# Kernel optimization log

Hardware: AMD Instinct MI355X
Metric: run time of the kernel (lower is better)

The kernel has to match this reference:

```python
import jax, jax.numpy as jnp
import numpy as np

EMBED_DIM = 512
K = 30
B, M, L = 64, 1024, 256

def setup_inputs() -> dict:
    key = jax.random.key(0)
    ks = jax.random.split(key, 7)
    s = 0.05  # small scale so tanh/softmax stay in a sane numeric range
    return {
        "V": jax.random.normal(ks[0], (B, EMBED_DIM, M), dtype=jnp.float32),
        "Q": jax.random.normal(ks[1], (B, L, EMBED_DIM), dtype=jnp.float32),
        "W_b": jax.random.normal(ks[2], (EMBED_DIM, EMBED_DIM), dtype=jnp.float32) * s,
        "W_v": jax.random.normal(ks[3], (K, EMBED_DIM), dtype=jnp.float32) * s,
        "W_q": jax.random.normal(ks[4], (K, EMBED_DIM), dtype=jnp.float32) * s,
        "w_hv": jax.random.normal(ks[5], (K, 1), dtype=jnp.float32) * s,
        "w_hq": jax.random.normal(ks[6], (K, 1), dtype=jnp.float32) * s,
    }

def reference(V, Q, W_b, W_v, W_q, w_hv, w_hq):
    # V: [B, d, M], Q: [B, L, d]
    b, d, m = V.shape
    l = Q.shape[1]
    WbV = jnp.einsum('de,bem->bdm', W_b, V)          # [B, d, M]
    C = jnp.matmul(Q, WbV)                            # affinity [B, L, M]
    WvV = jnp.einsum('kd,bdm->bkm', W_v, V)           # [B, k, M]
    WqQ = jnp.einsum('kd,bld->bkl', W_q, Q)           # [B, k, L]
    H_v = jnp.tanh(WvV + jnp.matmul(WqQ, C))          # [B, k, M]
    H_q = jnp.tanh(WqQ + jnp.matmul(WvV, jnp.swapaxes(C, 1, 2)))  # [B, k, L]
    a_v = jax.nn.softmax(jnp.einsum('ko,bkm->bom', w_hv, H_v), axis=2)  # [B, 1, M]
    a_q = jax.nn.softmax(jnp.einsum('ko,bkl->bol', w_hq, H_q), axis=2)  # [B, 1, L]
    # torch stacks a_v M times then matmuls -> M identical pooled rows; compute
    # the pooled vector once and broadcast (same math, no [B,M,M] intermediate).
    v1 = jnp.matmul(a_v, jnp.swapaxes(V, 1, 2))       # [B, 1, d]
    q1 = jnp.matmul(a_q, Q)                           # [B, 1, d]
    v = jnp.broadcast_to(v1, (b, m, d))               # [B, M, d]
    q = jnp.broadcast_to(q1, (b, l, d))               # [B, L, d]
    return (v, q)
```

## Files before the change

### kernel.cpp

```cpp
#include <hip/hip_runtime.h>

constexpr int Bn = 64;
constexpr int Dn = 512;
constexpr int Mn = 1024;
constexpr int Ln = 256;
constexpr int Kn = 30;
constexpr int KP = 32;

typedef __attribute__((ext_vector_type(4))) float f32x4;
typedef __attribute__((ext_vector_type(2))) float f32x2;
typedef __attribute__((ext_vector_type(4))) unsigned int u32x4;
typedef __attribute__((ext_vector_type(8))) _Float16 f16x8;
typedef __attribute__((ext_vector_type(2))) _Float16 f16x2;
typedef unsigned short ushort_t;

__device__ __forceinline__ void cvt_pair(float a, float b,
                                         unsigned int& hp, unsigned int& lp)
{
    _Float16 ha = (_Float16)a, hb = (_Float16)b;
    _Float16 la = (_Float16)(a - (float)ha), lb = (_Float16)(b - (float)hb);
    f16x2 hv = {ha, hb}, lv = {la, lb};
    hp = __builtin_bit_cast(unsigned int, hv);
    lp = __builtin_bit_cast(unsigned int, lv);
}

__device__ __forceinline__ unsigned int cvt_one_pack(float x)
{
    _Float16 h = (_Float16)x;
    _Float16 l = (_Float16)(x - (float)h);
    return (unsigned int)__builtin_bit_cast(ushort_t, l) |
           ((unsigned int)__builtin_bit_cast(ushort_t, h) << 16);
}

template <int MT, bool BT, int EPI>
__global__ __launch_bounds__(256) void fgemm_kernel(
    const float* __restrict__ A, const float* __restrict__ B,
    float* __restrict__ C,
    const float* __restrict__ Wvec, const float* __restrict__ Xadd,
    float* __restrict__ Yout,
    int Mreal, int Ndim, int Kdim, int ldA, int ldB,
    long sA, long sB, long sC)
{
    constexpr int BM = MT * 16;
    constexpr int AP = 20;
    constexpr int ASZ = BM * AP;
    constexpr int BP_NN = 66;
    constexpr int BSZ = BT ? (2 * 64 * AP) : (32 * BP_NN);
    __shared__ unsigned int smem[2 * ASZ + BSZ];
    __shared__ float wsh[32];
    unsigned int* Ah = smem;
    unsigned int* Al = smem + ASZ;
    unsigned int* Bh = smem + 2 * ASZ;
    unsigned int* Bl = Bh + 64 * AP;
    unsigned int* Bp = smem + 2 * ASZ;

    const int t  = threadIdx.x;
    const int n0 = blockIdx.x * 64;
    const int m0 = blockIdx.y * BM;
    const int b  = blockIdx.z;
    const float* Ab = A + (long)b * sA;
    const float* Bb = B + (long)b * sB;

    const int lane = t & 63, w = t >> 6;
    const int fr = lane & 15, g = lane >> 4;
    const int kp  = t & 15, r16 = t >> 4;
    const int nn  = t & 63, kr  = t >> 6;

    if (EPI >= 2 && t < 32) wsh[t] = (t < Kn) ? Wvec[t] : 0.f;

    float as[MT][2];
    float bsv[8];

    auto stageA = [&](int k0) {
        #pragma unroll
        for (int i = 0; i < MT; i++) {
            int gm = m0 + r16 + 16 * i;
            float x0 = 0.f, x1 = 0.f;
            if (gm < Mreal) {
                f32x2 v = *(const f32x2*)&Ab[(long)gm * ldA + k0 + 2 * kp];
                x0 = v.x; x1 = v.y;
            }
            as[i][0] = x0; as[i][1] = x1;
        }
    };
    auto stageB = [&](int k0) {
        if constexpr (BT) {
            #pragma unroll
            for (int i = 0; i < 4; i++) {
                f32x2 v = *(const f32x2*)&Bb[(long)(n0 + r16 + 16 * i) * ldB + k0 + 2 * kp];
                bsv[2 * i] = v.x; bsv[2 * i + 1] = v.y;
            }
        } else {
            #pragma unroll
            for (int i = 0; i < 8; i++)
                bsv[i] = Bb[(long)(k0 + kr + 4 * i) * ldB + n0 + nn];
        }
    };
    auto storeStage = [&]() {
        #pragma unroll
        for (int i = 0; i < MT; i++) {
            unsigned int hp, lp;
            cvt_pair(as[i][0], as[i][1], hp, lp);
            Ah[(r16 + 16 * i) * AP + kp] = hp;
            Al[(r16 + 16 * i) * AP + kp] = lp;
        }
        if constexpr (BT) {
            #pragma unroll
            for (int i = 0; i < 4; i++) {
                unsigned int hp, lp;
                cvt_pair(bsv[2 * i], bsv[2 * i + 1], hp, lp);
                Bh[(r16 + 16 * i) * AP + kp] = hp;
                Bl[(r16 + 16 * i) * AP + kp] = lp;
            }
        } else {
            #pragma unroll
            for (int i = 0; i < 8; i++)
                Bp[(kr + 4 * i) * BP_NN + nn] = cvt_one_pack(bsv[i]);
        }
    };

    f32x4 acc[MT];
    #pragma unroll
    for (int i = 0; i < MT; i++) acc[i] = (f32x4){0.f, 0.f, 0.f, 0.f};

    auto computeTile = [&]() {
        f16x8 fbh, fbl;
        if constexpr (BT) {
            int row = w * 16 + fr;
            fbh = __builtin_bit_cast(f16x8, *(const u32x4*)&Bh[row * AP + g * 4]);
            fbl = __builtin_bit_cast(f16x8, *(const u32x4*)&Bl[row * AP + g * 4]);
        } else {
            unsigned int p[8];
            #pragma unroll
            for (int j = 0; j < 8; j++)
                p[j] = Bp[(g * 8 + j) * BP_NN + w * 16 + fr];
            unsigned int hu[4], lu[4];
            #pragma unroll
            for (int r = 0; r < 4; r++) {
                hu[r] = __builtin_amdgcn_perm(p[2 * r + 1], p[2 * r], 0x07060302u);
                lu[r] = __builtin_amdgcn_perm(p[2 * r + 1], p[2 * r], 0x05040100u);
            }
            fbh = __builtin_bit_cast(f16x8, (u32x4){hu[0], hu[1], hu[2], hu[3]});
            fbl = __builtin_bit_cast(f16x8, (u32x4){lu[0], lu[1], lu[2], lu[3]});
        }
        #pragma unroll
        for (int mt = 0; mt < MT; mt++) {
            int row = fr + 16 * mt;
            f16x8 fah = __builtin_bit_cast(f16x8, *(const u32x4*)&Ah[row * AP + g * 4]);
            f16x8 fal = __builtin_bit_cast(f16x8, *(const u32x4*)&Al[row * AP + g * 4]);
            acc[mt] = __builtin_amdgcn_mfma_f32_16x16x32_f16(fah, fbh, acc[mt], 0, 0, 0);
            acc[mt] = __builtin_amdgcn_mfma_f32_16x16x32_f16(fal, fbh, acc[mt], 0, 0, 0);
            acc[mt] = __builtin_amdgcn_mfma_f32_16x16x32_f16(fah, fbl, acc[mt], 0, 0, 0);
        }
    };

    stageA(0); stageB(0);
    storeStage();
    __syncthreads();
    const int nt = Kdim >> 5;
    for (int tt = 0; tt < nt; tt++) {
        const bool more = (tt + 1 < nt);
        if (more) { stageA((tt + 1) * 32); stageB((tt + 1) * 32); }
        computeTile();
        if (more) {
            __syncthreads();
            storeStage();
            __syncthreads();
        }
    }

    const int col = n0 + w * 16 + fr;
    if constexpr (EPI == 0) {
        float* Cb = C + (long)b * sC;
        #pragma unroll
        for (int mt = 0; mt < MT; mt++)
            #pragma unroll
            for (int r = 0; r < 4; r++)
                Cb[(long)(m0 + mt * 16 + g * 4 + r) * Ndim + col] = acc[mt][r];
    } else if constexpr (EPI == 1) {
        #pragma unroll
        for (int mt = 0; mt < MT; mt++)
            #pragma unroll
            for (int r = 0; r < 4; r++) {
                int gr = m0 + mt * 16 + g * 4 + r;
                int sr = (gr >> 5) * 64 + 32 + (gr & 31);
                C[(long)sr * Ndim + col] = acc[mt][r];
            }
    } else if constexpr (EPI == 2) {
        float* Cb = C + (long)b * sC;
        float s = 0.f;
        #pragma unroll
        for (int mt = 0; mt < 2; mt++)
            #pragma unroll
            for (int r = 0; r < 4; r++) {
                int row = mt * 16 + g * 4 + r;
                Cb[(long)row * Ndim + col] = acc[mt][r];
                s += wsh[row] * tanhf(acc[mt][r] + acc[mt + 2][r]);
            }
        s += __shfl_xor(s, 16, 64);
        s += __shfl_xor(s, 32, 64);
        if (g == 0) Yout[(long)b * Ndim + col] = s;
    } else {
        const float* Xb = Xadd + (long)b * sC;
        float s = 0.f;
        #pragma unroll
        for (int mt = 0; mt < MT; mt++)
            #pragma unroll
            for (int r = 0; r < 4; r++) {
                int row = mt * 16 + g * 4 + r;
                s += wsh[row] * tanhf(Xb[(long)row * Ndim + col] + acc[mt][r]);
            }
        s += __shfl_xor(s, 16, 64);
        s += __shfl_xor(s, 32, 64);
        if (g == 0) Yout[(long)b * Ndim + col] = s;
    }
}

__global__ void prep_sa_kernel(const float* __restrict__ Wv,
                               float* __restrict__ Sa)
{
    const int b = blockIdx.x, t = threadIdx.x;
    for (int idx = t; idx < 32 * Dn; idx += 256) {
        int row = idx >> 9, col = idx & 511;
        Sa[((long)b * 64 + row) * Dn + col] =
            (row < Kn) ? Wv[(long)row * Dn + col] : 0.f;
    }
}

__global__ __launch_bounds__(1024) void smpool_v_kernel(
    const float* __restrict__ sv, const float* __restrict__ V,
    float* __restrict__ v1)
{
    const int b = blockIdx.y, qtr = blockIdx.x, t = threadIdx.x;
    const int wid = t >> 6, lane = t & 63;
    __shared__ float red[16];
    __shared__ float bc;
    __shared__ float av[Mn];

    float x = sv[(long)b * Mn + t];
    float v = x;
    #pragma unroll
    for (int off = 32; off > 0; off >>= 1) v = fmaxf(v, __shfl_down(v, off, 64));
    if (lane == 0) red[wid] = v;
    __syncthreads();
    if (t == 0) {
        float m = red[0];
        for (int i = 1; i < 16; i++) m = fmaxf(m, red[i]);
        bc = m;
    }
    __syncthreads();
    float e = expf(x - bc);
    v = e;
    #pragma unroll
    for (int off = 32; off > 0; off >>= 1) v += __shfl_down(v, off, 64);
    if (lane == 0) red[wid] = v;
    __syncthreads();
    if (t == 0) {
        float s = 0.f;
        for (int i = 0; i < 16; i++) s += red[i];
        bc = s;
    }
    __syncthreads();
    av[t] = e / bc;
    __syncthreads();

    f32x4 aa[4];
    #pragma unroll
    for (int i = 0; i < 4; i++) aa[i] = *(const f32x4*)&av[4 * (lane + 64 * i)];

    #pragma unroll
    for (int j = 0; j < 8; j++) {
        int e_ = qtr * 128 + wid * 8 + j;
        const float* vr = V + ((long)b * Dn + e_) * Mn;
        float acc = 0.f;
        #pragma unroll
        for (int i = 0; i < 4; i++) {
            f32x4 vv = *(const f32x4*)&vr[4 * (lane + 64 * i)];
            acc += vv.x * aa[i].x + vv.y * aa[i].y + vv.z * aa[i].z + vv.w * aa[i].w;
        }
        #pragma unroll
        for (int off = 32; off > 0; off >>= 1) acc += __shfl_down(acc, off, 64);
        if (lane == 0) v1[(long)b * Dn + e_] = acc;
    }
}

__global__ __launch_bounds__(256) void smpool_q_kernel(
    const float* __restrict__ sq, const float* __restrict__ Q,
    float* __restrict__ q1)
{
    const int b = blockIdx.y, half = blockIdx.x, t = threadIdx.x;
    const int wid = t >> 6, lane = t & 63;
    __shared__ float red[4];
    __shared__ float bc;
    __shared__ float aq[Ln];

    float x = sq[(long)b * Ln + t];
    float v = x;
    #pragma unroll
    for (int off = 32; off > 0; off >>= 1) v = fmaxf(v, __shfl_down(v, off, 64));
    if (lane == 0) red[wid] = v;
    __syncthreads();
    if (t == 0) {
        float m = red[0];
        for (int i = 1; i < 4; i++) m = fmaxf(m, red[i]);
        bc = m;
    }
    __syncthreads();
    float e = expf(x - bc);
    v = e;
    #pragma unroll
    for (int off = 32; off > 0; off >>= 1) v += __shfl_down(v, off, 64);
    if (lane == 0) red[wid] = v;
    __syncthreads();
    if (t == 0) {
        float s = 0.f;
        for (int i = 0; i < 4; i++) s += red[i];
        bc = s;
    }
    __syncthreads();
    aq[t] = e / bc;
    __syncthreads();

    const int e_ = half * 256 + t;
    const float* Qb = Q + (long)b * Ln * Dn;
    float acc = 0.f;
    #pragma unroll 4
    for (int l = 0; l < Ln; l++)
        acc += aq[l] * Qb[(long)l * Dn + e_];
    q1[(long)b * Dn + e_] = acc;
}

__global__ void bcast_kernel(const float* __restrict__ v1,
                             const float* __restrict__ q1,
                             float* __restrict__ out)
{
    const long nv4 = (long)Bn * Mn * Dn / 4;
    const long nq4 = (long)Bn * Ln * Dn / 4;
    long idx = (long)blockIdx.x * blockDim.x + threadIdx.x;
    float4* o4 = (float4*)out;
    if (idx < nv4) {
        long fidx = idx * 4;
        int e4 = (int)(fidx & (Dn - 1));
        long bm = fidx >> 9;
        int b = (int)(bm >> 10);
        o4[idx] = *(const float4*)(v1 + (long)b * Dn + e4);
    } else if (idx < nv4 + nq4) {
        long fidx = (idx - nv4) * 4;
        int e4 = (int)(fidx & (Dn - 1));
        long bl = fidx >> 9;
        int b = (int)(bl >> 8);
        o4[idx] = *(const float4*)(q1 + (long)b * Dn + e4);
    }
}


extern "C" void kernel_launch(void* const* d_in, const int* in_sizes, int n_in,
                              void* d_out, int out_size, void* d_ws, size_t ws_size,
                              hipStream_t stream)
{
    const float* V    = (const float*)d_in[0];
    const float* Q    = (const float*)d_in[1];
    const float* W_b  = (const float*)d_in[2];
    const float* W_v  = (const float*)d_in[3];
    const float* W_q  = (const float*)d_in[4];
    const float* w_hv = (const float*)d_in[5];
    const float* w_hq = (const float*)d_in[6];
    float* out = (float*)d_out;

    const long szWqQ = (long)Bn * KP * Ln;
    const long szU   = (long)Bn * KP * Dn;
    const long szSa  = (long)Bn * 64 * Dn;
    const long szSo  = (long)Bn * 32 * Mn;

    float* ws   = (float*)d_ws;
    float* WqQ  = ws;
    float* U    = WqQ + szWqQ;
    float* Sa   = U   + szU;
    float* Sout = Sa  + szSa;
    float* R    = Sout + szSo;
    float* G    = R   + szU;
    float* sv   = G   + szU;
    float* sq   = sv  + (long)Bn * Mn;
    float* v1   = sq  + (long)Bn * Ln;
    float* q1   = v1  + (long)Bn * Dn;

    prep_sa_kernel<<<Bn, 256, 0, stream>>>(W_v, Sa);

    fgemm_kernel<2, true, 0><<<dim3(Ln / 64, 1, Bn), 256, 0, stream>>>(
        W_q, Q, WqQ, nullptr, nullptr, nullptr,
        Kn, Ln, Dn, Dn, Dn, 0, (long)Ln * Dn, (long)KP * Ln);

    fgemm_kernel<2, false, 0><<<dim3(Dn / 64, 1, Bn), 256, 0, stream>>>(
        WqQ, Q, U, nullptr, nullptr, nullptr,
        KP, Dn, Ln, Ln, Dn, (long)KP * Ln, (long)Ln * Dn, (long)KP * Dn);

    fgemm_kernel<4, false, 1><<<dim3(Dn / 64, Bn * KP / 64, 1), 256, 0, stream>>>(
        U, W_b, Sa, nullptr, nullptr, nullptr,
        Bn * KP, Dn, Dn, Dn, Dn, 0, 0, 0);

    fgemm_kernel<4, false, 2><<<dim3(Mn / 64, 1, Bn), 256, 0, stream>>>(
        Sa, V, Sout, w_hv, nullptr, sv,
        64, Mn, Dn, Dn, Mn, (long)64 * Dn, (long)Dn * Mn, (long)32 * Mn);

    fgemm_kernel<2, true, 0><<<dim3(Dn / 64, 1, Bn), 256, 0, stream>>>(
        Sout, V, R, nullptr, nullptr, nullptr,
        KP, Dn, Mn, Mn, Mn, (long)32 * Mn, (long)Dn * Mn, (long)KP * Dn);

    fgemm_kernel<4, true, 0><<<dim3(Dn / 64, Bn * KP / 64, 1), 256, 0, stream>>>(
        R, W_b, G, nullptr, nullptr, nullptr,
        Bn * KP, Dn, Dn, Dn, Dn, 0, 0, 0);

    fgemm_kernel<2, true, 3><<<dim3(Ln / 64, 1, Bn), 256, 0, stream>>>(
        G, Q, nullptr, w_hq, WqQ, sq,
        KP, Ln, Dn, Dn, Dn, (long)KP * Dn, (long)Ln * Dn, (long)KP * Ln);

    smpool_v_kernel<<<dim3(4, Bn), 1024, 0, stream>>>(sv, V, v1);

    smpool_q_kernel<<<dim3(2, Bn), 256, 0, stream>>>(sq, Q, q1);

    {
        long n4 = (long)Bn * Mn * Dn / 4 + (long)Bn * Ln * Dn / 4;
        bcast_kernel<<<(int)((n4 + 255) / 256), 256, 0, stream>>>(v1, q1, out);
    }
}
```

Baseline: 494.6 us.

## Pre-pack fp16 hi/lo operands, double-buffer LDS, and parallelize q pooling

```diff
diff --git a/kernel.cpp b/kernel.cpp
--- a/kernel.cpp
+++ b/kernel.cpp
@@ -10,9 +10,25 @@
 typedef __attribute__((ext_vector_type(4))) float f32x4;
 typedef __attribute__((ext_vector_type(2))) float f32x2;
 typedef __attribute__((ext_vector_type(4))) unsigned int u32x4;
+typedef __attribute__((ext_vector_type(2))) unsigned int u32x2;
 typedef __attribute__((ext_vector_type(8))) _Float16 f16x8;
 typedef __attribute__((ext_vector_type(2))) _Float16 f16x2;
 typedef unsigned short ushort_t;
+
+__device__ __forceinline__ unsigned int cvt_one_pack(float x)
+{
+    _Float16 h = (_Float16)x;
+    _Float16 l = (_Float16)(x - (float)h);
+    return (unsigned int)__builtin_bit_cast(ushort_t, l) |
+           ((unsigned int)__builtin_bit_cast(ushort_t, h) << 16);
+}
+
+__device__ __forceinline__ float unpacksplit(unsigned int p)
+{
+    _Float16 h = __builtin_bit_cast(_Float16, (ushort_t)(p >> 16));
+    _Float16 l = __builtin_bit_cast(_Float16, (ushort_t)(p & 0xffffu));
+    return (float)h + (float)l;
+}
 
 __device__ __forceinline__ void cvt_pair(float a, float b,
                                          unsigned int& hp, unsigned int& lp)
@@ -24,19 +40,37 @@
     lp = __builtin_bit_cast(unsigned int, lv);
 }
 
-__device__ __forceinline__ unsigned int cvt_one_pack(float x)
-{
-    _Float16 h = (_Float16)x;
-    _Float16 l = (_Float16)(x - (float)h);
-    return (unsigned int)__builtin_bit_cast(ushort_t, l) |
-           ((unsigned int)__builtin_bit_cast(ushort_t, h) << 16);
-}
-
-template <int MT, bool BT, int EPI>
+#define PERM_HI 0x07060302u
+#define PERM_LO 0x05040100u
+
+__global__ __launch_bounds__(256) void pack4_kernel(
+    const float* __restrict__ s0, unsigned int* __restrict__ d0, long n0,
+    const float* __restrict__ s1, unsigned int* __restrict__ d1, long n1,
+    const float* __restrict__ s2, unsigned int* __restrict__ d2, long n2,
+    const float* __restrict__ s3, unsigned int* __restrict__ d3, long n3)
+{
+    long total4 = (n0 + n1 + n2 + n3) >> 2;
+    long stride = (long)gridDim.x * blockDim.x;
+    for (long c = (long)blockIdx.x * blockDim.x + threadIdx.x; c < total4; c += stride) {
+        long i = c * 4;
+        const float* s; unsigned int* d; long off;
+        if (i < n0)                { s = s0; d = d0; off = i; }
+        else if (i < n0 + n1)      { s = s1; d = d1; off = i - n0; }
+        else if (i < n0 + n1 + n2) { s = s2; d = d2; off = i - n0 - n1; }
+        else                       { s = s3; d = d3; off = i - n0 - n1 - n2; }
+        f32x4 v = *(const f32x4*)(s + off);
+        u32x4 o = { cvt_one_pack(v.x), cvt_one_pack(v.y),
+                    cvt_one_pack(v.z), cvt_one_pack(v.w) };
+        *(u32x4*)(d + off) = o;
+    }
+}
+
+template <int MT, bool BT, int EPI, bool BPACK, int ASRC>
 __global__ __launch_bounds__(256) void fgemm_kernel(
-    const float* __restrict__ A, const float* __restrict__ B,
-    float* __restrict__ C,
-    const float* __restrict__ Wvec, const float* __restrict__ Xadd,
+    const unsigned int* __restrict__ A, const void* __restrict__ B,
+    const unsigned int* __restrict__ A2,
+    unsigned int* __restrict__ C,
+    const float* __restrict__ Wvec, const unsigned int* __restrict__ Xadd,
     float* __restrict__ Yout,
     int Mreal, int Ndim, int Kdim, int ldA, int ldB,
     long sA, long sB, long sC)
@@ -46,20 +80,17 @@
     constexpr int ASZ = BM * AP;
     constexpr int BP_NN = 66;
     constexpr int BSZ = BT ? (2 * 64 * AP) : (32 * BP_NN);
-    __shared__ unsigned int smem[2 * ASZ + BSZ];
+    constexpr int HALF = 2 * ASZ + BSZ;
+    __shared__ unsigned int smem[2 * HALF];
     __shared__ float wsh[32];
-    unsigned int* Ah = smem;
-    unsigned int* Al = smem + ASZ;
-    unsigned int* Bh = smem + 2 * ASZ;
-    unsigned int* Bl = Bh + 64 * AP;
-    unsigned int* Bp = smem + 2 * ASZ;
 
     const int t  = threadIdx.x;
     const int n0 = blockIdx.x * 64;
     const int m0 = blockIdx.y * BM;
     const int b  = blockIdx.z;
-    const float* Ab = A + (long)b * sA;
-    const float* Bb = B + (long)b * sB;
+    const unsigned int* Ab = A + (long)b * sA;
+    const float*        Bf = (const float*)B + (long)b * sB;
+    const unsigned int* Bu = (const unsigned int*)B + (long)b * sB;
 
     const int lane = t & 63, w = t >> 6;
     const int fr = lane & 15, g = lane >> 4;
@@ -68,54 +99,82 @@
 
     if (EPI >= 2 && t < 32) wsh[t] = (t < Kn) ? Wvec[t] : 0.f;
 
-    float as[MT][2];
-    float bsv[8];
+    unsigned int aA[MT][2];
+    unsigned int bu[8];
+    float bf[8];
 
     auto stageA = [&](int k0) {
         #pragma unroll
         for (int i = 0; i < MT; i++) {
             int gm = m0 + r16 + 16 * i;
-            float x0 = 0.f, x1 = 0.f;
-            if (gm < Mreal) {
-                f32x2 v = *(const f32x2*)&Ab[(long)gm * ldA + k0 + 2 * kp];
-                x0 = v.x; x1 = v.y;
-            }
-            as[i][0] = x0; as[i][1] = x1;
+            unsigned int p0 = 0, p1 = 0;
+            if constexpr (ASRC == 2) {
+                if (gm < Kn) {
+                    u32x2 v = *(const u32x2*)&A[(long)gm * ldA + k0 + 2 * kp];
+                    p0 = v.x; p1 = v.y;
+                } else if (gm >= 32) {
+                    u32x2 v = *(const u32x2*)&A2[((long)b * 32 + gm - 32) * ldA + k0 + 2 * kp];
+                    p0 = v.x; p1 = v.y;
+                }
+            } else {
+                if (gm < Mreal) {
+                    u32x2 v = *(const u32x2*)&Ab[(long)gm * ldA + k0 + 2 * kp];
+                    p0 = v.x; p1 = v.y;
+                }
+            }
+            aA[i][0] = p0; aA[i][1] = p1;
         }
     };
     auto stageB = [&](int k0) {
         if constexpr (BT) {
             #pragma unroll
             for (int i = 0; i < 4; i++) {
-                f32x2 v = *(const f32x2*)&Bb[(long)(n0 + r16 + 16 * i) * ldB + k0 + 2 * kp];
-                bsv[2 * i] = v.x; bsv[2 * i + 1] = v.y;
+                long off = (long)(n0 + r16 + 16 * i) * ldB + k0 + 2 * kp;
+                if constexpr (BPACK) {
+                    u32x2 v = *(const u32x2*)&Bu[off];
+                    bu[2 * i] = v.x; bu[2 * i + 1] = v.y;
+                } else {
+                    f32x2 v = *(const f32x2*)&Bf[off];
+                    bf[2 * i] = v.x; bf[2 * i + 1] = v.y;
+                }
             }
         } else {
             #pragma unroll
-            for (int i = 0; i < 8; i++)
-                bsv[i] = Bb[(long)(k0 + kr + 4 * i) * ldB + n0 + nn];
+            for (int i = 0; i < 8; i++) {
+                long off = (long)(k0 + kr + 4 * i) * ldB + n0 + nn;
+                if constexpr (BPACK) bu[i] = Bu[off];
+                else                 bf[i] = Bf[off];
+            }
         }
     };
-    auto storeStage = [&]() {
+    auto storeStage = [&](unsigned int* sm) {
+        unsigned int* Ah = sm;
+        unsigned int* Al = sm + ASZ;
         #pragma unroll
         for (int i = 0; i < MT; i++) {
-            unsigned int hp, lp;
-            cvt_pair(as[i][0], as[i][1], hp, lp);
-            Ah[(r16 + 16 * i) * AP + kp] = hp;
-            Al[(r16 + 16 * i) * AP + kp] = lp;
+            Ah[(r16 + 16 * i) * AP + kp] = __builtin_amdgcn_perm(aA[i][1], aA[i][0], PERM_HI);
+            Al[(r16 + 16 * i) * AP + kp] = __builtin_amdgcn_perm(aA[i][1], aA[i][0], PERM_LO);
         }
         if constexpr (BT) {
+            unsigned int* Bh = sm + 2 * ASZ;
+            unsigned int* Bl = Bh + 64 * AP;
             #pragma unroll
             for (int i = 0; i < 4; i++) {
                 unsigned int hp, lp;
-                cvt_pair(bsv[2 * i], bsv[2 * i + 1], hp, lp);
+                if constexpr (BPACK) {
+                    hp = __builtin_amdgcn_perm(bu[2 * i + 1], bu[2 * i], PERM_HI);
+                    lp = __builtin_amdgcn_perm(bu[2 * i + 1], bu[2 * i], PERM_LO);
+                } else {
+                    cvt_pair(bf[2 * i], bf[2 * i + 1], hp, lp);
+                }
                 Bh[(r16 + 16 * i) * AP + kp] = hp;
                 Bl[(r16 + 16 * i) * AP + kp] = lp;
             }
         } else {
+            unsigned int* Bp = sm + 2 * ASZ;
             #pragma unroll
             for (int i = 0; i < 8; i++)
-                Bp[(kr + 4 * i) * BP_NN + nn] = cvt_one_pack(bsv[i]);
+                Bp[(kr + 4 * i) * BP_NN + nn] = BPACK ? bu[i] : cvt_one_pack(bf[i]);
         }
     };
 
@@ -123,13 +182,18 @@
     #pragma unroll
     for (int i = 0; i < MT; i++) acc[i] = (f32x4){0.f, 0.f, 0.f, 0.f};
 
-    auto computeTile = [&]() {
+    auto computeTile = [&](const unsigned int* sm) {
+        const unsigned int* Ah = sm;
+        const unsigned int* Al = sm + ASZ;
         f16x8 fbh, fbl;
         if constexpr (BT) {
+            const unsigned int* Bh = sm + 2 * ASZ;
+            const unsigned int* Bl = Bh + 64 * AP;
             int row = w * 16 + fr;
             fbh = __builtin_bit_cast(f16x8, *(const u32x4*)&Bh[row * AP + g * 4]);
             fbl = __builtin_bit_cast(f16x8, *(const u32x4*)&Bl[row * AP + g * 4]);
         } else {
+            const unsigned int* Bp = sm + 2 * ASZ;
             unsigned int p[8];
             #pragma unroll
             for (int j = 0; j < 8; j++)
@@ -137,8 +201,8 @@
             unsigned int hu[4], lu[4];
             #pragma unroll
             for (int r = 0; r < 4; r++) {
-                hu[r] = __builtin_amdgcn_perm(p[2 * r + 1], p[2 * r], 0x07060302u);
-                lu[r] = __builtin_amdgcn_perm(p[2 * r + 1], p[2 * r], 0x05040100u);
+                hu[r] = __builtin_amdgcn_perm(p[2 * r + 1], p[2 * r], PERM_HI);
+                lu[r] = __builtin_amdgcn_perm(p[2 * r + 1], p[2 * r], PERM_LO);
             }
             fbh = __builtin_bit_cast(f16x8, (u32x4){hu[0], hu[1], hu[2], hu[3]});
             fbl = __builtin_bit_cast(f16x8, (u32x4){lu[0], lu[1], lu[2], lu[3]});
@@ -154,76 +218,56 @@
         }
     };
 
+    const int nt = Kdim >> 5;
     stageA(0); stageB(0);
-    storeStage();
-    __syncthreads();
-    const int nt = Kdim >> 5;
+    storeStage(smem);
+    __syncthreads();
     for (int tt = 0; tt < nt; tt++) {
+        unsigned int* cur = smem + (tt & 1) * HALF;
+        unsigned int* nxt = smem + ((tt + 1) & 1) * HALF;
         const bool more = (tt + 1 < nt);
-        if (more) { stageA((tt + 1) * 32); stageB((tt + 1) * 32); }
-        computeTile();
-        if (more) {
-            __syncthreads();
-            storeStage();
-            __syncthreads();
-        }
+        if (more) { stageA((tt + 1) << 5); stageB((tt + 1) << 5); }
+        computeTile(cur);
+        if (more) storeStage(nxt);
+        __syncthreads();
     }
 
     const int col = n0 + w * 16 + fr;
     if constexpr (EPI == 0) {
-        float* Cb = C + (long)b * sC;
+        unsigned int* Cb = C + (long)b * sC;
         #pragma unroll
         for (int mt = 0; mt < MT; mt++)
             #pragma unroll
             for (int r = 0; r < 4; r++)
-                Cb[(long)(m0 + mt * 16 + g * 4 + r) * Ndim + col] = acc[mt][r];
-    } else if constexpr (EPI == 1) {
-        #pragma unroll
-        for (int mt = 0; mt < MT; mt++)
-            #pragma unroll
-            for (int r = 0; r < 4; r++) {
-                int gr = m0 + mt * 16 + g * 4 + r;
-                int sr = (gr >> 5) * 64 + 32 + (gr & 31);
-                C[(long)sr * Ndim + col] = acc[mt][r];
-            }
+                Cb[(long)(m0 + mt * 16 + g * 4 + r) * Ndim + col] = cvt_one_pack(acc[mt][r]);
     } else if constexpr (EPI == 2) {
-        float* Cb = C + (long)b * sC;
+        unsigned int* Cb = C + (long)b * sC;
         float s = 0.f;
         #pragma unroll
         for (int mt = 0; mt < 2; mt++)
             #pragma unroll
             for (int r = 0; r < 4; r++) {
                 int row = mt * 16 + g * 4 + r;
-                Cb[(long)row * Ndim + col] = acc[mt][r];
+                Cb[(long)row * Ndim + col] = cvt_one_pack(acc[mt][r]);
                 s += wsh[row] * tanhf(acc[mt][r] + acc[mt + 2][r]);
             }
         s += __shfl_xor(s, 16, 64);
         s += __shfl_xor(s, 32, 64);
         if (g == 0) Yout[(long)b * Ndim + col] = s;
     } else {
-        const float* Xb = Xadd + (long)b * sC;
+        const unsigned int* Xb = Xadd + (long)b * sC;
         float s = 0.f;
         #pragma unroll
         for (int mt = 0; mt < MT; mt++)
             #pragma unroll
             for (int r = 0; r < 4; r++) {
                 int row = mt * 16 + g * 4 + r;
-                s += wsh[row] * tanhf(Xb[(long)row * Ndim + col] + acc[mt][r]);
+                float x = unpacksplit(Xb[(long)row * Ndim + col]);
+                s += wsh[row] * tanhf(x + acc[mt][r]);
             }
         s += __shfl_xor(s, 16, 64);
         s += __shfl_xor(s, 32, 64);
         if (g == 0) Yout[(long)b * Ndim + col] = s;
-    }
-}
-
-__global__ void prep_sa_kernel(const float* __restrict__ Wv,
-                               float* __restrict__ Sa)
-{
-    const int b = blockIdx.x, t = threadIdx.x;
-    for (int idx = t; idx < 32 * Dn; idx += 256) {
-        int row = idx >> 9, col = idx & 511;
-        Sa[((long)b * 64 + row) * Dn + col] =
-            (row < Kn) ? Wv[(long)row * Dn + col] : 0.f;
     }
 }
 
@@ -288,7 +332,7 @@
     const float* __restrict__ sq, const float* __restrict__ Q,
     float* __restrict__ q1)
 {
-    const int b = blockIdx.y, half = blockIdx.x, t = threadIdx.x;
+    const int b = blockIdx.y, eb = blockIdx.x, t = threadIdx.x;
     const int wid = t >> 6, lane = t & 63;
     __shared__ float red[4];
     __shared__ float bc;
@@ -321,13 +365,17 @@
     aq[t] = e / bc;
     __syncthreads();
 
-    const int e_ = half * 256 + t;
+    const int e_ = eb * 64 + (t >> 2), qtr = t & 3;
     const float* Qb = Q + (long)b * Ln * Dn;
     float acc = 0.f;
     #pragma unroll 4
-    for (int l = 0; l < Ln; l++)
+    for (int i = 0; i < 64; i++) {
+        int l = qtr * 64 + i;
         acc += aq[l] * Qb[(long)l * Dn + e_];
-    q1[(long)b * Dn + e_] = acc;
+    }
+    acc += __shfl_xor(acc, 1, 64);
+    acc += __shfl_xor(acc, 2, 64);
+    if (qtr == 0) q1[(long)b * Dn + e_] = acc;
 }
 
 __global__ void bcast_kernel(const float* __restrict__ v1,
@@ -367,56 +415,63 @@
     const float* w_hq = (const float*)d_in[6];
     float* out = (float*)d_out;
 
+    const long nQ  = (long)Bn * Ln * Dn;
+    const long nWb = (long)Dn * Dn;
+    const long nWq = (long)Kn * Dn;
+    const long nWv = (long)Kn * Dn;
     const long szWqQ = (long)Bn * KP * Ln;
     const long szU   = (long)Bn * KP * Dn;
-    const long szSa  = (long)Bn * 64 * Dn;
-    const long szSo  = (long)Bn * 32 * Mn;
-
-    float* ws   = (float*)d_ws;
-    float* WqQ  = ws;
-    float* U    = WqQ + szWqQ;
-    float* Sa   = U   + szU;
-    float* Sout = Sa  + szSa;
-    float* R    = Sout + szSo;
-    float* G    = R   + szU;
-    float* sv   = G   + szU;
-    float* sq   = sv  + (long)Bn * Mn;
-    float* v1   = sq  + (long)Bn * Ln;
-    float* q1   = v1  + (long)Bn * Dn;
-
-    prep_sa_kernel<<<Bn, 256, 0, stream>>>(W_v, Sa);
-
-    fgemm_kernel<2, true, 0><<<dim3(Ln / 64, 1, Bn), 256, 0, stream>>>(
-        W_q, Q, WqQ, nullptr, nullptr, nullptr,
+    const long szSo  = (long)Bn * KP * Mn;
+
+    unsigned int* wsu   = (unsigned int*)d_ws;
+    unsigned int* Qp    = wsu;
+    unsigned int* Wbp   = Qp    + nQ;
+    unsigned int* Wqp   = Wbp   + nWb;
+    unsigned int* Wvp   = Wqp   + nWq;
+    unsigned int* WqQp  = Wvp   + nWv;
+    unsigned int* Up    = WqQp  + szWqQ;
+    unsigned int* Pp    = Up    + szU;
+    unsigned int* Soutp = Pp    + szU;
+    unsigned int* Rp    = Soutp + szSo;
+    unsigned int* Gp    = Rp    + szU;
+    float* sv = (float*)(Gp + szU);
+    float* sq = sv + (long)Bn * Mn;
+    float* v1 = sq + (long)Bn * Ln;
+    float* q1 = v1 + (long)Bn * Dn;
+
+    pack4_kernel<<<4096, 256, 0, stream>>>(
+        Q, Qp, nQ, W_b, Wbp, nWb, W_q, Wqp, nWq, W_v, Wvp, nWv);
+
+    fgemm_kernel<2, true, 0, true, 0><<<dim3(4, 1, 64), 256, 0, stream>>>(
+        Wqp, Qp, nullptr, WqQp, nullptr, nullptr, nullptr,
         Kn, Ln, Dn, Dn, Dn, 0, (long)Ln * Dn, (long)KP * Ln);
 
-    fgemm_kernel<2, false, 0><<<dim3(Dn / 64, 1, Bn), 256, 0, stream>>>(
-        WqQ, Q, U, nullptr, nullptr, nullptr,
+    fgemm_kernel<2, false, 0, true, 0><<<dim3(8, 1, 64), 256, 0, stream>>>(
+        WqQp, Qp, nullptr, Up, nullptr, nullptr, nullptr,
         KP, Dn, Ln, Ln, Dn, (long)KP * Ln, (long)Ln * Dn, (long)KP * Dn);
 
-    fgemm_kernel<4, false, 1><<<dim3(Dn / 64, Bn * KP / 64, 1), 256, 0, stream>>>(
-        U, W_b, Sa, nullptr, nullptr, nullptr,
+    fgemm_kernel<4, false, 0, true, 0><<<dim3(8, 32, 1), 256, 0, stream>>>(
+        Up, Wbp, nullptr, Pp, nullptr, nullptr, nullptr,
         Bn * KP, Dn, Dn, Dn, Dn, 0, 0, 0);
 
-    fgemm_kernel<4, false, 2><<<dim3(Mn / 64, 1, Bn), 256, 0, stream>>>(
-        Sa, V, Sout, w_hv, nullptr, sv,
-        64, Mn, Dn, Dn, Mn, (long)64 * Dn, (long)Dn * Mn, (long)32 * Mn);
-
-    fgemm_kernel<2, true, 0><<<dim3(Dn / 64, 1, Bn), 256, 0, stream>>>(
-        Sout, V, R, nullptr, nullptr, nullptr,
-        KP, Dn, Mn, Mn, Mn, (long)32 * Mn, (long)Dn * Mn, (long)KP * Dn);
-
-    fgemm_kernel<4, true, 0><<<dim3(Dn / 64, Bn * KP / 64, 1), 256, 0, stream>>>(
-        R, W_b, G, nullptr, nullptr, nullptr,
+    fgemm_kernel<4, false, 2, false, 2><<<dim3(16, 1, 64), 256, 0, stream>>>(
+        Wvp, V, Pp, Soutp, w_hv, nullptr, sv,
+        64, Mn, Dn, Dn, Mn, 0, (long)Dn * Mn, (long)KP * Mn);
+
+    fgemm_kernel<2, true, 0, false, 0><<<dim3(8, 1, 64), 256, 0, stream>>>(
+        Soutp, V, nullptr, Rp, nullptr, nullptr, nullptr,
+        KP, Dn, Mn, Mn, Mn, (long)KP * Mn, (long)Dn * Mn, (long)KP * Dn);
+
+    fgemm_kernel<4, true, 0, true, 0><<<dim3(8, 32, 1), 256, 0, stream>>>(
+        Rp, Wbp, nullptr, Gp, nullptr, nullptr, nullptr,
         Bn * KP, Dn, Dn, Dn, Dn, 0, 0, 0);
 
-    fgemm_kernel<2, true, 3><<<dim3(Ln / 64, 1, Bn), 256, 0, stream>>>(
-        G, Q, nullptr, w_hq, WqQ, sq,
+    fgemm_kernel<2, true, 3, true, 0><<<dim3(4, 1, 64), 256, 0, stream>>>(
+        Gp, Qp, nullptr, nullptr, w_hq, WqQp, sq,
         KP, Ln, Dn, Dn, Dn, (long)KP * Dn, (long)Ln * Dn, (long)KP * Ln);
 
     smpool_v_kernel<<<dim3(4, Bn), 1024, 0, stream>>>(sv, V, v1);
-
-    smpool_q_kernel<<<dim3(2, Bn), 256, 0, stream>>>(sq, Q, q1);
+    smpool_q_kernel<<<dim3(8, Bn), 256, 0, stream>>>(sq, Q, q1);
 
     {
         long n4 = (long)Bn * Mn * Dn / 4 + (long)Bn * Ln * Dn / 4;
```

Result: faster. 451.8 us (-8.6%).
